# Kernel tuning notes

Measured on AMD Instinct MI355X. Metric: run time of the kernel, lower is better.

## Reference

```python
import jax, jax.numpy as jnp
import numpy as np
from math import comb

B = 1024                 # num_batch
NUM, NVAR, NUM_OBS = 100, 11, 10
T_FIN = 15.0
K_P = 20.0; K_D = 2.0 * np.sqrt(20.0); K_P_V = 20.0
A_OBS, B_OBS = 8.0, 4.2
RHO_V, RHO_PROJ, RHO_LANE, RHO_OBS, RHO_OFFSET, RHO_INEQ = 1.0, 1.0, 100.0, 100.0, 1.0, 100.0
V_MIN, V_MAX, A_MAX = 0.1, 30.0, 8.0
MAXITER = 20
LATENT, HID, INP_DIM, TRAJ_DIM = 2, 1024, 55, 200


def _bernstein():
    # degree-10 Bernstein polynomial basis on [0, T_FIN], sampled at NUM points
    n = NVAR - 1
    s = np.linspace(0.0, 1.0, NUM)
    bm = lambda m: np.stack([comb(m, k) * s**k * (1.0 - s)**(m - k) for k in range(m + 1)], 1)
    P, B9, B8 = bm(n), bm(n - 1), bm(n - 2)
    Z = np.zeros(NUM)
    Pdot = np.stack([(n / T_FIN) * ((B9[:, k - 1] if k >= 1 else Z) - (B9[:, k] if k <= n - 1 else Z)) for k in range(n + 1)], 1)
    Pddot = np.stack([(n * (n - 1) / T_FIN**2) * ((B8[:, k - 2] if k >= 2 else Z) - 2.0 * (B8[:, k - 1] if 1 <= k <= n - 1 else Z) + (B8[:, k] if k <= n - 2 else Z)) for k in range(n + 1)], 1)
    return tuple(jnp.asarray(a, jnp.float32) for a in (P, Pdot, Pddot))


def _forward(inp, initial_state_ego, traj_gt, y_ub, y_lb, eps,
             enc_w1, enc_b1, enc_w2, enc_b2, enc_wmu, enc_bmu, enc_wlv, enc_blv,
             dec_w1, dec_b1, dec_w2, dec_b2, dec_w3, dec_b3,
             P, Pdot, Pddot, inp_mean, inp_std):
    Bn = inp.shape[0]
    tot_time = jnp.linspace(0.0, T_FIN, NUM)

    # ---- cVAE encode / reparameterize / decode ----
    inp_n = (inp - inp_mean) / inp_std
    h = jax.nn.relu(jnp.concatenate([inp_n, traj_gt], 1) @ enc_w1 + enc_b1)
    h = jax.nn.relu(h @ enc_w2 + enc_b2)
    mu = h @ enc_wmu + enc_bmu
    logvar = h @ enc_wlv + enc_blv
    z = mu + jnp.exp(0.5 * logvar) * eps
    h = jax.nn.relu(jnp.concatenate([z, inp_n], 1) @ dec_w1 + dec_b1)
    h = jax.nn.relu(h @ dec_w2 + dec_b2)
    nn_out = h @ dec_w3 + dec_b3          # (B, 8): 4 v_des + 4 y_des setpoints

    # ---- constant constraint matrices ----
    A_eq_x = jnp.stack([P[0], Pdot[0], Pddot[0]])                 # (3, 11)
    A_eq_y = jnp.stack([P[0], Pdot[0], Pddot[0], Pdot[-1]])       # (4, 11)
    A_pd = Pddot - K_P * P - K_D * Pdot
    A_vd = Pddot - K_P_V * Pdot
    cost_smooth = Pddot.T @ Pddot
    I = jnp.eye(NVAR, dtype=P.dtype)

    def kkt_inv(cost, A_eq):
        m = A_eq.shape[0]
        M = jnp.block([[cost, A_eq.T], [A_eq, jnp.zeros((m, m), cost.dtype)]])
        return jnp.linalg.inv(M)

    # ---- boundary conditions ----
    zb = jnp.zeros((Bn,), inp.dtype)
    b_eq_x = jnp.stack([zb, initial_state_ego[:, 2], zb], 1)
    b_eq_y = jnp.stack([zb, initial_state_ego[:, 3], zb, zb], 1)

    # ---- QP layer 1 (behavioral layer) ----
    # sum_i A_vd_i^T A_vd_i over the 4 row-partitions == A_vd^T A_vd
    cost1_x = cost_smooth + RHO_V * (A_vd.T @ A_vd)
    cost1_y = cost_smooth + RHO_OFFSET * (A_pd.T @ A_pd)
    inv1_x = kkt_inv(cost1_x, A_eq_x)
    inv1_y = kkt_inv(cost1_y, A_eq_y)
    v_des = jnp.repeat(nn_out[:, 0:4], NUM // 4, axis=1)   # (B, 100) piecewise setpoints
    y_des = jnp.repeat(nn_out[:, 4:8], NUM // 4, axis=1)
    lincost_x1 = -RHO_V * ((-K_P_V * v_des) @ A_vd)
    lincost_y1 = -RHO_OFFSET * ((-K_P * y_des) @ A_pd)
    c_x_bar = (jnp.concatenate([-lincost_x1, b_eq_x], 1) @ inv1_x.T)[:, :NVAR]
    c_y_bar = (jnp.concatenate([-lincost_y1, b_eq_y], 1) @ inv1_y.T)[:, :NVAR]

    # ---- obstacle constant-velocity rollouts (obstacle-major, matches tile(P)) ----
    x_obs, y_obs = inp[:, 5::5], inp[:, 6::5]
    vx_obs, vy_obs = inp[:, 7::5], inp[:, 8::5]
    x_obs_traj = (x_obs[:, :, None] + vx_obs[:, :, None] * tot_time).reshape(Bn, NUM_OBS * NUM)
    y_obs_traj = (y_obs[:, :, None] + vy_obs[:, :, None] * tot_time).reshape(Bn, NUM_OBS * NUM)

    # ---- QP layer 2 (iterative ADMM-style projection) ----
    A_obs_m = jnp.tile(P, (NUM_OBS, 1))          # (1000, 11)
    A_lane = jnp.vstack([P, -P])                 # (200, 11)
    A_vel, A_acc = Pdot, Pddot
    cost2_x = RHO_PROJ * I + RHO_OBS * (A_obs_m.T @ A_obs_m) + RHO_INEQ * (A_acc.T @ A_acc) + RHO_INEQ * (A_vel.T @ A_vel)
    cost2_y = cost2_x + RHO_LANE * (A_lane.T @ A_lane)
    inv2_x = kkt_inv(cost2_x, A_eq_x)
    inv2_y = kkt_inv(cost2_y, A_eq_y)
    ones_num = jnp.ones((1, NUM), inp.dtype)
    b_lane = jnp.concatenate([y_ub[:, None] * ones_num, -y_lb[:, None] * ones_num], 1)  # (B, 200)

    def step(carry, _):
        primal, lx, ly = carry
        cx, cy = primal[:, :NVAR], primal[:, NVAR:]
        x, xdot, xddot = cx @ P.T, cx @ Pdot.T, cx @ Pddot.T
        y, ydot, yddot = cy @ P.T, cy @ Pdot.T, cy @ Pddot.T
        # obstacle polar decomposition
        wc = jnp.tile(x, (1, NUM_OBS)) - x_obs_traj
        ws = jnp.tile(y, (1, NUM_OBS)) - y_obs_traj
        a_o = jnp.arctan2(A_OBS * ws, B_OBS * wc)
        ca, sa = jnp.cos(a_o), jnp.sin(a_o)
        c1 = RHO_OBS * (A_OBS**2 * ca**2 + B_OBS**2 * sa**2)
        c2 = RHO_OBS * (A_OBS * wc * ca + B_OBS * ws * sa)
        d_o = jnp.maximum(1.0, c2 / c1)
        # velocity / acceleration polar decomposition with box clipping
        a_v = jnp.arctan2(ydot, xdot)
        cv, sv = jnp.cos(a_v), jnp.sin(a_v)
        d_v = jnp.clip(xdot * cv + ydot * sv, V_MIN, V_MAX)
        a_a = jnp.arctan2(yddot, xddot)
        caa, saa = jnp.cos(a_a), jnp.sin(a_a)
        d_a = jnp.clip(xddot * caa + yddot * saa, 0.0, A_MAX)
        # lane slack
        lane_proj = cy @ A_lane.T
        s_lane = jnp.maximum(0.0, b_lane - lane_proj)
        res_lane = lane_proj - b_lane + s_lane
        # residuals -> dual updates
        rxo = wc - A_OBS * d_o * ca
        ryo = ws - B_OBS * d_o * sa
        rvx, rvy = xdot - d_v * cv, ydot - d_v * sv
        rax, ray = xddot - d_a * caa, yddot - d_a * saa
        lx = lx - RHO_OBS * (rxo @ A_obs_m) - RHO_INEQ * (rax @ A_acc) - RHO_INEQ * (rvx @ A_vel)
        ly = ly - RHO_OBS * (ryo @ A_obs_m) - RHO_INEQ * (ray @ A_acc) - RHO_INEQ * (rvy @ A_vel) - RHO_LANE * (res_lane @ A_lane)
        # linear cost + batched KKT solve via precomputed inverse
        b_ox = x_obs_traj + A_OBS * d_o * ca
        b_oy = y_obs_traj + B_OBS * d_o * sa
        lin_x = -lx - RHO_PROJ * c_x_bar - RHO_OBS * (b_ox @ A_obs_m) - RHO_INEQ * ((d_a * caa) @ A_acc) - RHO_INEQ * ((d_v * cv) @ A_vel)
        lin_y = -ly - RHO_PROJ * c_y_bar - RHO_OBS * (b_oy @ A_obs_m) - RHO_INEQ * ((d_a * saa) @ A_acc) - RHO_INEQ * ((d_v * sv) @ A_vel) - RHO_LANE * ((b_lane - s_lane) @ A_lane)
        sx = (jnp.concatenate([-lin_x, b_eq_x], 1) @ inv2_x.T)[:, :NVAR]
        sy = (jnp.concatenate([-lin_y, b_eq_y], 1) @ inv2_y.T)[:, :NVAR]
        return (jnp.concatenate([sx, sy], 1), lx, ly), None

    primal0 = jnp.concatenate([c_x_bar, c_y_bar], 1)
    lam0 = jnp.zeros((Bn, NVAR), inp.dtype)
    (primal, _, _), _ = jax.lax.scan(step, (primal0, lam0, lam0), None, length=MAXITER)
    return primal  # (B, 2*NVAR) projected trajectory coefficients


def setup_inputs() -> dict:
    key = jax.random.key(0)
    ks = jax.random.split(key, 16)
    P, Pdot, Pddot = _bernstein()
    n = lambda k, sh, sc=1.0: sc * jax.random.normal(k, sh, jnp.float32)
    return {
        "inp": n(ks[0], (B, INP_DIM), 5.0),
        "initial_state_ego": jnp.concatenate([jnp.zeros((B, 2), jnp.float32), 10.0 + n(ks[1], (B, 2))], 1),
        "traj_gt": n(ks[2], (B, TRAJ_DIM)),
        "y_ub": jnp.full((B,), 3.5, jnp.float32),
        "y_lb": jnp.full((B,), -3.5, jnp.float32),
        "eps": n(ks[3], (B, LATENT)),
        "enc_w1": n(ks[4], (INP_DIM + TRAJ_DIM, HID), 0.05), "enc_b1": jnp.zeros((HID,), jnp.float32),
        "enc_w2": n(ks[5], (HID, HID), 0.03), "enc_b2": jnp.zeros((HID,), jnp.float32),
        "enc_wmu": n(ks[6], (HID, LATENT), 0.03), "enc_bmu": jnp.zeros((LATENT,), jnp.float32),
        "enc_wlv": n(ks[7], (HID, LATENT), 0.03), "enc_blv": jnp.zeros((LATENT,), jnp.float32),
        "dec_w1": n(ks[8], (LATENT + INP_DIM, HID), 0.05), "dec_b1": jnp.zeros((HID,), jnp.float32),
        "dec_w2": n(ks[9], (HID, HID), 0.03), "dec_b2": jnp.zeros((HID,), jnp.float32),
        "dec_w3": n(ks[10], (HID, 8), 0.03), "dec_b3": jnp.zeros((8,), jnp.float32),
        "P": P, "Pdot": Pdot, "Pddot": Pddot,
        "inp_mean": jnp.zeros((INP_DIM,), jnp.float32),
        "inp_std": jnp.ones((INP_DIM,), jnp.float32),
    }


def reference(inp, initial_state_ego, traj_gt, y_ub, y_lb, eps,
              enc_w1, enc_b1, enc_w2, enc_b2, enc_wmu, enc_bmu, enc_wlv, enc_blv,
              dec_w1, dec_b1, dec_w2, dec_b2, dec_w3, dec_b3,
              P, Pdot, Pddot, inp_mean, inp_std):
    return _forward(inp, initial_state_ego, traj_gt, y_ub, y_lb, eps,
                    enc_w1, enc_b1, enc_w2, enc_b2, enc_wmu, enc_bmu, enc_wlv, enc_blv,
                    dec_w1, dec_b1, dec_w2, dec_b2, dec_w3, dec_b3,
                    P, Pdot, Pddot, inp_mean, inp_std)
```

## Files before the change

### kernel.cpp

```cpp
#include <hip/hip_runtime.h>
#include <hip/hip_bf16.h>
#include <math.h>

#define BATCH   1024
#define NUMPT   100
#define NVAR    11
#define NOBS    10
#define HID     1024
#define INPD    55
#define TRAJD   200

#define T_FIN_C   15.0f
#define K_P_C     20.0f
#define K_D_C     8.944271909999159f
#define K_P_V_C   20.0f
#define A_OBS_C   8.0f
#define B_OBS_C   4.2f
#define AB_C      33.6f
#define ABSQ_C    1128.96f
#define RHO_V_C      1.0f
#define RHO_PROJ_C   1.0f
#define RHO_LANE_C   100.0f
#define RHO_OBS_C    100.0f
#define RHO_OFFSET_C 1.0f
#define RHO_INEQ_C   100.0f
#define V_MIN_C   0.1f
#define V_MAX_C   30.0f
#define A_MAX_C   8.0f
#define MAXIT     20

#define WS_INV1X  0
#define WS_INV1Y  256
#define WS_INV2X  512
#define WS_INV2Y  768
#define WS_SVD    1024
#define WS_SPD    1088
#define WS_QX     1152
#define WS_QY     1280
#define WS_R2X    1408
#define WS_R2Y    1536
#define WS_BIG    2048

typedef __bf16 bf16x8 __attribute__((ext_vector_type(8)));
typedef float  f32x4  __attribute__((ext_vector_type(4)));

__global__ __launch_bounds__(256) void setup_kernel(
    const float* __restrict__ Pg, const float* __restrict__ Pdg,
    const float* __restrict__ Pddg, float* __restrict__ ws,
    const float* __restrict__ inp, const float* __restrict__ traj,
    const float* __restrict__ mean, const float* __restrict__ stdv,
    __bf16* __restrict__ enc_in, __bf16* __restrict__ dec_in,
    const float* __restrict__ w1, const float* __restrict__ w2,
    const float* __restrict__ w3, const float* __restrict__ w4,
    __bf16* __restrict__ o1, __bf16* __restrict__ o2,
    __bf16* __restrict__ o3, __bf16* __restrict__ o4)
{
    __shared__ float sP[NUMPT*NVAR], sPd[NUMPT*NVAR], sPdd[NUMPT*NVAR];
    __shared__ float aug[15][31];
    __shared__ float fcol[15];
    __shared__ float sQ[121];
    __shared__ float sn[INPD];
    __shared__ float tile[64][65];
    __shared__ float s_pivinv;
    __shared__ int   s_pidx;
    const int tid = threadIdx.x, bid = blockIdx.x;

    if (bid >= 1028) {
        const int tb = bid - 1028;
        int wsel, kt, nt;
        if (tb < 64)       { wsel = 0; kt = tb >> 4;        nt = tb & 15; }
        else if (tb < 320) { wsel = 1; kt = (tb-64) >> 4;   nt = (tb-64) & 15; }
        else if (tb < 352) { wsel = 2; kt = (tb-320) >> 4;  nt = (tb-320) & 15; }
        else               { wsel = 3; kt = (tb-352) >> 4;  nt = (tb-352) & 15; }
        const float* W = (wsel==0) ? w1 : (wsel==1) ? w2 : (wsel==2) ? w3 : w4;
        __bf16* O      = (wsel==0) ? o1 : (wsel==1) ? o2 : (wsel==2) ? o3 : o4;
        const int K  = (wsel==0) ? 255 : (wsel==2) ? 57 : 1024;
        const int Kp = (wsel==0) ? 256 : (wsel==2) ? 128 : 1024;
        if (kt*64 >= Kp) return;
        const int k0 = kt*64, n0 = nt*64;
        const int rr = tid >> 6, c = tid & 63;
        #pragma unroll 4
        for (int it = 0; it < 16; ++it) {
            const int r = it*4 + rr;
            tile[r][c] = (k0 + r < K) ? W[(size_t)(k0 + r)*HID + n0 + c] : 0.0f;
        }
        __syncthreads();
        #pragma unroll 4
        for (int it = 0; it < 16; ++it) {
            const int r = it*4 + rr;
            O[(size_t)(n0 + r)*Kp + k0 + c] = (__bf16)tile[c][r];
        }
        return;
    }

    if (bid >= 4) {
        const int b = bid - 4;
        if (tid < INPD) {
            const float v = (inp[b*INPD + tid] - mean[tid]) / stdv[tid];
            sn[tid] = v;
            enc_in[b*256 + tid] = (__bf16)v;
        } else if (tid < 255) {
            enc_in[b*256 + tid] = (__bf16)traj[b*TRAJD + (tid - INPD)];
        } else {
            enc_in[b*256 + 255] = (__bf16)0.0f;
        }
        __syncthreads();
        if (tid >= 2 && tid < 128)
            dec_in[b*128 + tid] = (__bf16)((tid < 57) ? sn[tid - 2] : 0.0f);
        return;
    }

    for (int i = tid; i < NUMPT*NVAR; i += 256) {
        sP[i] = Pg[i]; sPd[i] = Pdg[i]; sPdd[i] = Pddg[i];
    }
    for (int i = tid; i < 15*31; i += 256) (&aug[0][0])[i] = 0.0f;
    __syncthreads();

    const int N = (bid == 0 || bid == 2) ? 14 : 15;

    if (tid < 121) {
        const int i = tid / 11, j = tid % 11;
        float s = 0.0f;
        if (bid == 0) {
            for (int t = 0; t < NUMPT; ++t) {
                float pdd_i = sPdd[t*NVAR+i], pdd_j = sPdd[t*NVAR+j];
                float av_i = pdd_i - K_P_V_C * sPd[t*NVAR+i];
                float av_j = pdd_j - K_P_V_C * sPd[t*NVAR+j];
                s += pdd_i*pdd_j + RHO_V_C * av_i*av_j;
            }
        } else if (bid == 1) {
            for (int t = 0; t < NUMPT; ++t) {
                float pdd_i = sPdd[t*NVAR+i], pdd_j = sPdd[t*NVAR+j];
                float ap_i = pdd_i - K_P_C*sP[t*NVAR+i] - K_D_C*sPd[t*NVAR+i];
                float ap_j = pdd_j - K_P_C*sP[t*NVAR+j] - K_D_C*sPd[t*NVAR+j];
                s += pdd_i*pdd_j + RHO_OFFSET_C * ap_i*ap_j;
            }
        } else {
            float obs_w = RHO_OBS_C * (float)NOBS;
            if (bid == 3) obs_w += RHO_LANE_C * 2.0f;
            for (int t = 0; t < NUMPT; ++t) {
                float p_i = sP[t*NVAR+i],   p_j = sP[t*NVAR+j];
                float pd_i = sPd[t*NVAR+i], pd_j = sPd[t*NVAR+j];
                float pdd_i = sPdd[t*NVAR+i], pdd_j = sPdd[t*NVAR+j];
                s += obs_w*p_i*p_j + RHO_INEQ_C*(pdd_i*pdd_j + pd_i*pd_j);
            }
            if (i == j) s += RHO_PROJ_C;
        }
        aug[i][j] = s;
    }
    if (tid < 11) {
        const int i = tid;
        float a0 = sP[i], a1 = sPd[i], a2 = sPdd[i];
        aug[i][11] = a0; aug[11][i] = a0;
        aug[i][12] = a1; aug[12][i] = a1;
        aug[i][13] = a2; aug[13][i] = a2;
        if (N == 15) { float a3 = sPd[99*NVAR + i]; aug[i][14] = a3; aug[14][i] = a3; }
    }
    if (tid < N) aug[tid][N + tid] = 1.0f;

    if (bid == 0 && tid < 44) {
        const int c = tid / 11, k = tid % 11;
        float sv = 0.0f, sp = 0.0f;
        for (int t = 25*c; t < 25*c + 25; ++t) {
            float p = sP[t*NVAR+k], pd = sPd[t*NVAR+k], pdd = sPdd[t*NVAR+k];
            sv += pdd - K_P_V_C * pd;
            sp += pdd - K_P_C * p - K_D_C * pd;
        }
        ws[WS_SVD + tid] = sv;
        ws[WS_SPD + tid] = sp;
    }
    __syncthreads();

    if ((bid == 2 || bid == 3) && tid < 121) {
        float v = aug[tid/11][tid%11];
        if (tid/11 == tid%11) v -= RHO_PROJ_C;
        sQ[tid] = v;
        ws[(bid == 2 ? WS_QX : WS_QY) + tid] = v;
    }

    for (int k = 0; k < N; ++k) {
        if (tid == 0) {
            int p = k; float best = fabsf(aug[k][k]);
            for (int i = k+1; i < N; ++i) {
                float v = fabsf(aug[i][k]);
                if (v > best) { best = v; p = i; }
            }
            s_pidx = p;
        }
        __syncthreads();
        const int p = s_pidx;
        if (p != k && tid < 2*N) {
            float tmp = aug[k][tid]; aug[k][tid] = aug[p][tid]; aug[p][tid] = tmp;
        }
        __syncthreads();
        if (tid == 0) s_pivinv = 1.0f / aug[k][k];
        __syncthreads();
        if (tid < 2*N) aug[k][tid] *= s_pivinv;
        __syncthreads();
        if (tid < N) fcol[tid] = (tid == k) ? 0.0f : aug[tid][k];
        __syncthreads();
        for (int idx = tid; idx < N*2*N; idx += 256) {
            const int i = idx / (2*N), j = idx % (2*N);
            if (i != k) aug[i][j] = fmaf(-fcol[i], aug[k][j], aug[i][j]);
        }
        __syncthreads();
    }

    float* dst = ws + (bid == 0 ? WS_INV1X : bid == 1 ? WS_INV1Y
                      : bid == 2 ? WS_INV2X : WS_INV2Y);
    for (int idx = tid; idx < N*N; idx += 256)
        dst[idx] = aug[idx / N][N + idx % N];
    __syncthreads();

    if ((bid == 2 || bid == 3) && tid < 121) {
        const int k = tid / 11, j = tid % 11;
        float a = 0.0f;
        #pragma unroll
        for (int m = 0; m < 11; ++m) a = fmaf(aug[k][N + m], sQ[m*11 + j], a);
        ws[(bid == 2 ? WS_R2X : WS_R2Y) + tid] = a;
    }
}

#define GEMM_CORE(A_, Wt_, Kp_, ...)                                          \
    __shared__ __bf16 As[32][136];                                            \
    __shared__ __bf16 Bs[64][136];                                            \
    const int tid = threadIdx.x;                                              \
    const int lane = tid & 63, wv = tid >> 6;                                 \
    const int wm = (wv >> 1) * 16, wn = (wv & 1) * 32;                        \
    const int ln = lane & 15, q = lane >> 4;                                  \
    const int row0 = blockIdx.y * 32, col0 = blockIdx.x * 64;                 \
    const int r16 = tid >> 4, ch = (tid & 15) * 8;                            \
    f32x4 acc0 = (f32x4){0,0,0,0}, acc1 = (f32x4){0,0,0,0};                   \
    for (int k0 = 0; k0 < (Kp_); k0 += 128) {                                 \
        bf16x8 va = *(const bf16x8*)&(A_)[(size_t)(row0 + r16)*(Kp_) + k0 + ch]; \
        bf16x8 vb = *(const bf16x8*)&(A_)[(size_t)(row0 + r16 + 16)*(Kp_) + k0 + ch]; \
        __VA_ARGS__                                                           \
        *(bf16x8*)&As[r16][ch] = va;                                          \
        *(bf16x8*)&As[r16 + 16][ch] = vb;                                     \
        _Pragma("unroll")                                                     \
        for (int p = 0; p < 4; ++p)                                           \
            *(bf16x8*)&Bs[r16 + 16*p][ch] =                                   \
                *(const bf16x8*)&(Wt_)[(size_t)(col0 + r16 + 16*p)*(Kp_) + k0 + ch]; \
        __syncthreads();                                                      \
        _Pragma("unroll")                                                     \
        for (int kc = 0; kc < 4; ++kc) {                                      \
            const bf16x8 a  = *(const bf16x8*)&As[wm + ln][kc*32 + q*8];      \
            const bf16x8 b0 = *(const bf16x8*)&Bs[wn + ln][kc*32 + q*8];      \
            const bf16x8 b1 = *(const bf16x8*)&Bs[wn + 16 + ln][kc*32 + q*8]; \
            acc0 = __builtin_amdgcn_mfma_f32_16x16x32_bf16(a, b0, acc0, 0, 0, 0); \
            acc1 = __builtin_amdgcn_mfma_f32_16x16x32_bf16(a, b1, acc1, 0, 0, 0); \
        }                                                                     \
        __syncthreads();                                                      \
    }

#define GEMM_WRITE_RELU(C_)                                                   \
    _Pragma("unroll")                                                         \
    for (int ni = 0; ni < 2; ++ni) {                                          \
        const int col = col0 + wn + ni*16 + ln;                               \
        const float bv = bias[col];                                           \
        const f32x4 av = ni ? acc1 : acc0;                                    \
        _Pragma("unroll")                                                     \
        for (int r = 0; r < 4; ++r) {                                         \
            const int row = row0 + wm + q*4 + r;                              \
            (C_)[(size_t)row * HID + col] = (__bf16)fmaxf(av[r] + bv, 0.0f);  \
        }                                                                     \
    }

__global__ __launch_bounds__(256) void gemm_relu(
    const __bf16* __restrict__ A, const __bf16* __restrict__ Wt,
    const float* __restrict__ bias, __bf16* __restrict__ C, int Kp)
{
    GEMM_CORE(A, Wt, Kp)
    GEMM_WRITE_RELU(C)
}

__global__ __launch_bounds__(256) void gemm_mulv(
    const __bf16* __restrict__ A, const __bf16* __restrict__ Wt,
    const float* __restrict__ bias,
    const float* __restrict__ wmu, const float* __restrict__ wlv,
    float* __restrict__ pmulv, int Kp)
{
    GEMM_CORE(A, Wt, Kp)
    const int c0 = col0 + wn + ln;
    const int c1 = c0 + 16;
    const float b0v = bias[c0], b1v = bias[c1];
    const float wm00 = wmu[c0*2+0], wm01 = wmu[c0*2+1];
    const float wm10 = wmu[c1*2+0], wm11 = wmu[c1*2+1];
    const float wl00 = wlv[c0*2+0], wl01 = wlv[c0*2+1];
    const float wl10 = wlv[c1*2+0], wl11 = wlv[c1*2+1];
    float pr[4][4];
    #pragma unroll
    for (int r = 0; r < 4; ++r) {
        const float h0 = fmaxf(acc0[r] + b0v, 0.0f);
        const float h1 = fmaxf(acc1[r] + b1v, 0.0f);
        pr[r][0] = fmaf(h0, wm00, h1*wm10);
        pr[r][1] = fmaf(h0, wm01, h1*wm11);
        pr[r][2] = fmaf(h0, wl00, h1*wl10);
        pr[r][3] = fmaf(h0, wl01, h1*wl11);
    }
    #pragma unroll
    for (int m = 1; m <= 8; m <<= 1)
        #pragma unroll
        for (int r = 0; r < 4; ++r)
            #pragma unroll
            for (int j = 0; j < 4; ++j)
                pr[r][j] += __shfl_xor(pr[r][j], m);
    if (ln == 0) {
        const int part = blockIdx.x*2 + (wv & 1);
        #pragma unroll
        for (int r = 0; r < 4; ++r) {
            const int row = row0 + wm + q*4 + r;
            *(float4*)&pmulv[(size_t)row*128 + part*4] =
                make_float4(pr[r][0], pr[r][1], pr[r][2], pr[r][3]);
        }
    }
}

__global__ __launch_bounds__(256) void gemm_zfix(
    const __bf16* __restrict__ A, const __bf16* __restrict__ Wt,
    const float* __restrict__ bias, __bf16* __restrict__ C, int Kp,
    const float* __restrict__ pmulv, const float* __restrict__ bmu,
    const float* __restrict__ blv, const float* __restrict__ eps)
{
    GEMM_CORE(A, Wt, Kp,
        if (ch == 0 && k0 == 0) {
            const int ra = row0 + r16;
            const int rb = ra + 16;
            float4 sa = make_float4(0.0f, 0.0f, 0.0f, 0.0f);
            float4 sb = make_float4(0.0f, 0.0f, 0.0f, 0.0f);
            for (int p = 0; p < 32; ++p) {
                const float4 qa = *(const float4*)&pmulv[(size_t)ra*128 + p*4];
                const float4 qb = *(const float4*)&pmulv[(size_t)rb*128 + p*4];
                sa.x += qa.x; sa.y += qa.y; sa.z += qa.z; sa.w += qa.w;
                sb.x += qb.x; sb.y += qb.y; sb.z += qb.z; sb.w += qb.w;
            }
            va[0] = (__bf16)fmaf(expf(0.5f*(sa.z + blv[0])), eps[ra*2+0], sa.x + bmu[0]);
            va[1] = (__bf16)fmaf(expf(0.5f*(sa.w + blv[1])), eps[ra*2+1], sa.y + bmu[1]);
            vb[0] = (__bf16)fmaf(expf(0.5f*(sb.z + blv[0])), eps[rb*2+0], sb.x + bmu[0]);
            vb[1] = (__bf16)fmaf(expf(0.5f*(sb.w + blv[1])), eps[rb*2+1], sb.y + bmu[1]);
        }
    )
    GEMM_WRITE_RELU(C)
}

__global__ __launch_bounds__(256) void gemm_out8(
    const __bf16* __restrict__ A, const __bf16* __restrict__ Wt,
    const float* __restrict__ bias, const float* __restrict__ w3,
    float* __restrict__ pnn, int Kp)
{
    GEMM_CORE(A, Wt, Kp)
    const int c0 = col0 + wn + ln;
    const int c1 = c0 + 16;
    const float b0v = bias[c0], b1v = bias[c1];
    float pr[4][8];
    #pragma unroll
    for (int r = 0; r < 4; ++r) {
        const float h0 = fmaxf(acc0[r] + b0v, 0.0f);
        const float h1 = fmaxf(acc1[r] + b1v, 0.0f);
        #pragma unroll
        for (int j = 0; j < 8; ++j)
            pr[r][j] = fmaf(h0, w3[c0*8 + j], h1*w3[c1*8 + j]);
    }
    #pragma unroll
    for (int m = 1; m <= 8; m <<= 1)
        #pragma unroll
        for (int r = 0; r < 4; ++r)
            #pragma unroll
            for (int j = 0; j < 8; ++j)
                pr[r][j] += __shfl_xor(pr[r][j], m);
    if (ln == 0) {
        const int part = blockIdx.x*2 + (wv & 1);
        #pragma unroll
        for (int r = 0; r < 4; ++r) {
            const int row = row0 + wm + q*4 + r;
            *(float4*)&pnn[(size_t)row*256 + part*8] =
                make_float4(pr[r][0], pr[r][1], pr[r][2], pr[r][3]);
            *(float4*)&pnn[(size_t)row*256 + part*8 + 4] =
                make_float4(pr[r][4], pr[r][5], pr[r][6], pr[r][7]);
        }
    }
}

#define DOT11(bb, a0, a1, a2) \
    fmaf(bb[0],a0.x, fmaf(bb[1],a0.y, fmaf(bb[2],a0.z, fmaf(bb[3],a0.w, \
    fmaf(bb[4],a1.x, fmaf(bb[5],a1.y, fmaf(bb[6],a1.z, fmaf(bb[7],a1.w, \
    fmaf(bb[8],a2.x, fmaf(bb[9],a2.y, bb[10]*a2.z))))))))))

__global__ __launch_bounds__(256) void solver_kernel(
    const float* __restrict__ pnn, const float* __restrict__ b3,
    const float* __restrict__ inp,
    const float* __restrict__ ise, const float* __restrict__ yub_p,
    const float* __restrict__ ylb_p,
    const float* __restrict__ Pg, const float* __restrict__ Pdg,
    const float* __restrict__ Pddg,
    const float* __restrict__ ws, float* __restrict__ out)
{
    __shared__ __align__(16) float sBcol[3][11][108];
    __shared__ float s_i2x[196], s_i2y[225], sR2x[121], sR2y[121];
    __shared__ __align__(16) float rows[7][104];
    __shared__ float dval[2][80];
    __shared__ __align__(16) float cxs[12], cys[12];
    __shared__ float wlin[24];
    __shared__ float obsS[4][10];
    __shared__ float nnS[8];

    const int tid = threadIdx.x;
    const int e = blockIdx.x;

    for (int i = tid; i < 3*11*108; i += 256) {
        const int mat = i / 1188, rem = i - mat*1188;
        const int k = rem / 108, t = rem - k*108;
        const float* G = (mat == 0) ? Pg : (mat == 1 ? Pdg : Pddg);
        sBcol[mat][k][t] = (t < NUMPT) ? G[t*NVAR + k] : 0.0f;
    }
    for (int i = tid; i < 196; i += 256) s_i2x[i] = ws[WS_INV2X + i];
    for (int i = tid; i < 225; i += 256) s_i2y[i] = ws[WS_INV2Y + i];
    for (int i = tid; i < 121; i += 256) { sR2x[i] = ws[WS_R2X + i]; sR2y[i] = ws[WS_R2Y + i]; }
    if (tid >= 200 && tid < 240) {
        const int i = tid - 200;
        obsS[i/10][i%10] = inp[e*INPD + 5 + (i/10) + 5*(i%10)];
    }
    if (tid >= 240 && tid < 248) {
        const int j = tid - 240;
        float s = b3[j];
        for (int p = 0; p < 32; ++p) s += pnn[(size_t)e*256 + p*8 + j];
        nnS[j] = s;
    }
    if (tid >= 64 && tid < 92) {
        const int i = tid - 64;
        rows[i >> 2][100 + (i & 3)] = 0.0f;
    }
    if (tid == 92) cxs[11] = 0.0f;
    if (tid == 93) cys[11] = 0.0f;

    const bool isA = (tid < 200);
    const int tA = tid >> 1, hA = tid & 1;
    const bool isB = (tid < 154);
    const int hB = (tid >= 77) ? 1 : 0;
    const int dB = tid - 77*hB;
    const int rB = dB / 11, kB = dB - 11*rB;
    const int mB = (rB==1||rB==4) ? 2 : ((rB==2||rB==5) ? 1 : 0);
    const float* colp = &sBcol[mB][kB][hB*52];
    const float* rowp = &rows[rB][hB*52];

    float bP[NVAR], bQ[NVAR];
    if (isA) {
        const float* Qsrc = hA ? Pddg : Pdg;
        #pragma unroll
        for (int k = 0; k < NVAR; ++k) {
            bP[k] = Pg[tA*NVAR+k];
            bQ[k] = Qsrc[tA*NVAR+k];
        }
    }

    const float vx0 = ise[e*4 + 2], vy0 = ise[e*4 + 3];
    const float yub = yub_p[e], ylb = ylb_p[e];
    __syncthreads();

    const float DT = T_FIN_C / 99.0f;
    float xo[5], yo[5];
    if (isA) {
        const int ob0 = 5*hA;
        #pragma unroll
        for (int o = 0; o < 5; ++o) {
            xo[o] = fmaf(obsS[2][ob0+o], tA*DT, obsS[0][ob0+o]);
            yo[o] = fmaf(obsS[3][ob0+o], tA*DT, obsS[1][ob0+o]);
        }
    }

    if (tid < 11) {
        float s = 0;
        #pragma unroll
        for (int c = 0; c < 4; ++c)
            s = fmaf(nnS[c], ws[WS_SVD + c*11 + tid], s);
        wlin[tid] = RHO_V_C * K_P_V_C * s;
    } else if (tid < 22) {
        const int k = tid - 11;
        float s = 0;
        #pragma unroll
        for (int c = 0; c < 4; ++c)
            s = fmaf(nnS[4 + c], ws[WS_SPD + c*11 + k], s);
        wlin[tid] = RHO_OFFSET_C * K_P_C * s;
    }
    __syncthreads();

    float lam = 0.0f, cb = 0.0f;
    if (tid < 11) {
        const int k = tid;
        float a = vx0 * ws[WS_INV1X + k*14 + 12];
        #pragma unroll
        for (int j = 0; j < NVAR; ++j)
            a = fmaf(-wlin[j], ws[WS_INV1X + k*14 + j], a);
        cb = a; cxs[k] = a;
    } else if (tid < 22) {
        const int k = tid - 11;
        float a = vy0 * ws[WS_INV1Y + k*15 + 12];
        #pragma unroll
        for (int j = 0; j < NVAR; ++j)
            a = fmaf(-wlin[11 + j], ws[WS_INV1Y + k*15 + j], a);
        cb = a; cys[k] = a;
    }
    __syncthreads();

    for (int it = 0; it < MAXIT; ++it) {
        if (isA) {
            const float4 x0 = *(const float4*)&cxs[0];
            const float4 x1 = *(const float4*)&cxs[4];
            const float4 x2 = *(const float4*)&cxs[8];
            const float4 y0 = *(const float4*)&cys[0];
            const float4 y1 = *(const float4*)&cys[4];
            const float4 y2 = *(const float4*)&cys[8];
            const float px = DOT11(bP, x0, x1, x2);
            const float py = DOT11(bP, y0, y1, y2);
            const float qx = DOT11(bQ, x0, x1, x2);
            const float qy = DOT11(bQ, y0, y1, y2);

            float srx = 0.0f, sry = 0.0f;
            #pragma unroll
            for (int o = 0; o < 5; ++o) {
                const float wc = px - xo[o], wsv = py - yo[o];
                const float aw = A_OBS_C * wsv, bw = B_OBS_C * wc;
                const float r2 = aw*aw + bw*bw;
                if (r2 > 0.0f) {
                    const float f = (r2 < ABSQ_C) ? (1.0f - AB_C * rsqrtf(r2)) : 0.0f;
                    srx = fmaf(wc, f, srx);
                    sry = fmaf(wsv, f, sry);
                } else {
                    srx -= A_OBS_C;
                }
            }
            const float mrx = srx + __shfl_xor(srx, 1);
            const float mry = sry + __shfl_xor(sry, 1);

            if (hA == 0) {
                rows[0][tA] = mrx;
                rows[3][tA] = mry;
                const float rv2 = qx*qx + qy*qy;
                float vxr, vyr;
                if (rv2 > 0.0f) {
                    const float ri = rsqrtf(rv2);
                    const float dv = fminf(fmaxf(rv2*ri, V_MIN_C), V_MAX_C);
                    const float f = 1.0f - dv*ri;
                    vxr = qx*f; vyr = qy*f;
                } else { vxr = -V_MIN_C; vyr = 0.0f; }
                rows[2][tA] = vxr;  rows[5][tA] = vyr;
                rows[6][tA] = fmaxf(0.0f, py - yub) - fmaxf(0.0f, ylb - py);
            } else {
                const float ra2 = qx*qx + qy*qy;
                float axr = 0.0f, ayr = 0.0f;
                if (ra2 > A_MAX_C*A_MAX_C) {
                    const float ri = rsqrtf(ra2);
                    const float f = 1.0f - A_MAX_C*ri;
                    axr = qx*f; ayr = qy*f;
                }
                rows[1][tA] = axr;  rows[4][tA] = ayr;
            }
        }
        __syncthreads();

        if (isB) {
            float s0 = 0.0f, s1 = 0.0f;
            #pragma unroll
            for (int i = 0; i < 13; ++i) {
                const float4 rr = *(const float4*)&rowp[i*4];
                const float4 cc = *(const float4*)&colp[i*4];
                s0 = fmaf(rr.x, cc.x, s0); s1 = fmaf(rr.y, cc.y, s1);
                s0 = fmaf(rr.z, cc.z, s0); s1 = fmaf(rr.w, cc.w, s1);
            }
            dval[hB][dB] = s0 + s1;
        }
        __syncthreads();

        if (tid < 22) {
            const int k = (tid < 11) ? tid : tid - 11;
            float u;
            if (tid < 11)
                u = RHO_OBS_C * ((dval[0][k]      + dval[1][k])
                               + (dval[0][11 + k] + dval[1][11 + k])
                               + (dval[0][22 + k] + dval[1][22 + k]));
            else
                u = RHO_OBS_C * ((dval[0][33 + k] + dval[1][33 + k])
                               + (dval[0][44 + k] + dval[1][44 + k])
                               + (dval[0][55 + k] + dval[1][55 + k])
                               + (dval[0][66 + k] + dval[1][66 + k]));
            wlin[tid] = 2.0f*u - lam - cb;
            lam -= u;
        }
        __builtin_amdgcn_wave_barrier();
        if (tid < 22) {
            const int k = (tid < 11) ? tid : tid - 11;
            if (tid < 11) {
                float a = vx0 * s_i2x[k*14 + 12];
                #pragma unroll
                for (int j = 0; j < NVAR; ++j) {
                    a = fmaf(-wlin[j], s_i2x[k*14 + j], a);
                    a = fmaf(sR2x[k*11 + j], cxs[j], a);
                }
                cxs[k] = a;
            } else {
                float a = vy0 * s_i2y[k*15 + 12];
                #pragma unroll
                for (int j = 0; j < NVAR; ++j) {
                    a = fmaf(-wlin[11 + j], s_i2y[k*15 + j], a);
                    a = fmaf(sR2y[k*11 + j], cys[j], a);
                }
                cys[k] = a;
            }
        }
        __syncthreads();
    }

    if (tid < NVAR) {
        out[e*22 + tid]      = cxs[tid];
        out[e*22 + 11 + tid] = cys[tid];
    }
}

extern "C" void kernel_launch(void* const* d_in, const int* in_sizes, int n_in,
                              void* d_out, int out_size, void* d_ws, size_t ws_size,
                              hipStream_t stream)
{
    (void)in_sizes; (void)n_in; (void)out_size; (void)ws_size;
    const float* inp    = (const float*)d_in[0];
    const float* ise    = (const float*)d_in[1];
    const float* traj   = (const float*)d_in[2];
    const float* yub    = (const float*)d_in[3];
    const float* ylb    = (const float*)d_in[4];
    const float* eps    = (const float*)d_in[5];
    const float* enc_w1 = (const float*)d_in[6];
    const float* enc_b1 = (const float*)d_in[7];
    const float* enc_w2 = (const float*)d_in[8];
    const float* enc_b2 = (const float*)d_in[9];
    const float* wmu    = (const float*)d_in[10];
    const float* bmu    = (const float*)d_in[11];
    const float* wlv    = (const float*)d_in[12];
    const float* blv    = (const float*)d_in[13];
    const float* dec_w1 = (const float*)d_in[14];
    const float* dec_b1 = (const float*)d_in[15];
    const float* dec_w2 = (const float*)d_in[16];
    const float* dec_b2 = (const float*)d_in[17];
    const float* dec_w3 = (const float*)d_in[18];
    const float* dec_b3 = (const float*)d_in[19];
    const float* P      = (const float*)d_in[20];
    const float* Pd     = (const float*)d_in[21];
    const float* Pdd    = (const float*)d_in[22];
    const float* mean   = (const float*)d_in[23];
    const float* stdv   = (const float*)d_in[24];

    float* ws    = (float*)d_ws;
    float* pmulv = ws + WS_BIG;
    float* pnn   = pmulv + (size_t)BATCH*128;
    __bf16* bfb  = (__bf16*)(pnn + (size_t)BATCH*256);
    __bf16* enc_in = bfb;
    __bf16* dec_in = enc_in + (size_t)BATCH*256;
    __bf16* hA     = dec_in + (size_t)BATCH*128;
    __bf16* wt1    = hA + (size_t)BATCH*HID;
    __bf16* wt2    = wt1 + (size_t)HID*256;
    __bf16* wt3    = wt2 + (size_t)HID*HID;
    __bf16* wt4    = wt3 + (size_t)HID*128;
    float* outf = (float*)d_out;

    setup_kernel<<<4 + 1024 + 608, 256, 0, stream>>>(
        P, Pd, Pdd, ws, inp, traj, mean, stdv, enc_in, dec_in,
        enc_w1, enc_w2, dec_w1, dec_w2, wt1, wt2, wt3, wt4);

    dim3 g(16, 32);
    gemm_relu<<<g, 256, 0, stream>>>(enc_in, wt1, enc_b1, hA, 256);
    gemm_mulv<<<g, 256, 0, stream>>>(hA, wt2, enc_b2, wmu, wlv, pmulv, 1024);
    gemm_zfix<<<g, 256, 0, stream>>>(dec_in, wt3, dec_b1, hA, 128,
                                     pmulv, bmu, blv, eps);
    gemm_out8<<<g, 256, 0, stream>>>(hA, wt4, dec_b2, dec_w3, pnn, 1024);
    solver_kernel<<<BATCH, 256, 0, stream>>>(pnn, dec_b3, inp, ise, yub, ylb,
                                             P, Pd, Pdd, ws, outf);
}
```

Measured before the change: 218.2 us.

## Fuse setup and four GEMM kernels into one persistent kernel with grid barriers

Merges the setup kernel (constant KKT inverses, input normalization, weight transposes) and the four MLP GEMM launches into a single 512-block persistent kernel. Stages are separated by atomic-counter grid barriers, and the counters are reset by a memset before launch. This removes kernel launch gaps and tail effects between the small stages. In exchange it relies on all 512 blocks being co-resident to avoid deadlock, and adds spin-wait barrier overhead.

```diff
diff --git a/kernel.cpp b/kernel.cpp
--- a/kernel.cpp
+++ b/kernel.cpp
@@ -39,197 +39,27 @@
 #define WS_QY     1280
 #define WS_R2X    1408
 #define WS_R2Y    1536
+#define WS_CTR    1700
 #define WS_BIG    2048
 
 typedef __bf16 bf16x8 __attribute__((ext_vector_type(8)));
 typedef float  f32x4  __attribute__((ext_vector_type(4)));
 
-__global__ __launch_bounds__(256) void setup_kernel(
-    const float* __restrict__ Pg, const float* __restrict__ Pdg,
-    const float* __restrict__ Pddg, float* __restrict__ ws,
-    const float* __restrict__ inp, const float* __restrict__ traj,
-    const float* __restrict__ mean, const float* __restrict__ stdv,
-    __bf16* __restrict__ enc_in, __bf16* __restrict__ dec_in,
-    const float* __restrict__ w1, const float* __restrict__ w2,
-    const float* __restrict__ w3, const float* __restrict__ w4,
-    __bf16* __restrict__ o1, __bf16* __restrict__ o2,
-    __bf16* __restrict__ o3, __bf16* __restrict__ o4)
-{
-    __shared__ float sP[NUMPT*NVAR], sPd[NUMPT*NVAR], sPdd[NUMPT*NVAR];
-    __shared__ float aug[15][31];
-    __shared__ float fcol[15];
-    __shared__ float sQ[121];
-    __shared__ float sn[INPD];
-    __shared__ float tile[64][65];
-    __shared__ float s_pivinv;
-    __shared__ int   s_pidx;
-    const int tid = threadIdx.x, bid = blockIdx.x;
-
-    if (bid >= 1028) {
-        const int tb = bid - 1028;
-        int wsel, kt, nt;
-        if (tb < 64)       { wsel = 0; kt = tb >> 4;        nt = tb & 15; }
-        else if (tb < 320) { wsel = 1; kt = (tb-64) >> 4;   nt = (tb-64) & 15; }
-        else if (tb < 352) { wsel = 2; kt = (tb-320) >> 4;  nt = (tb-320) & 15; }
-        else               { wsel = 3; kt = (tb-352) >> 4;  nt = (tb-352) & 15; }
-        const float* W = (wsel==0) ? w1 : (wsel==1) ? w2 : (wsel==2) ? w3 : w4;
-        __bf16* O      = (wsel==0) ? o1 : (wsel==1) ? o2 : (wsel==2) ? o3 : o4;
-        const int K  = (wsel==0) ? 255 : (wsel==2) ? 57 : 1024;
-        const int Kp = (wsel==0) ? 256 : (wsel==2) ? 128 : 1024;
-        if (kt*64 >= Kp) return;
-        const int k0 = kt*64, n0 = nt*64;
-        const int rr = tid >> 6, c = tid & 63;
-        #pragma unroll 4
-        for (int it = 0; it < 16; ++it) {
-            const int r = it*4 + rr;
-            tile[r][c] = (k0 + r < K) ? W[(size_t)(k0 + r)*HID + n0 + c] : 0.0f;
-        }
-        __syncthreads();
-        #pragma unroll 4
-        for (int it = 0; it < 16; ++it) {
-            const int r = it*4 + rr;
-            O[(size_t)(n0 + r)*Kp + k0 + c] = (__bf16)tile[c][r];
-        }
-        return;
-    }
-
-    if (bid >= 4) {
-        const int b = bid - 4;
-        if (tid < INPD) {
-            const float v = (inp[b*INPD + tid] - mean[tid]) / stdv[tid];
-            sn[tid] = v;
-            enc_in[b*256 + tid] = (__bf16)v;
-        } else if (tid < 255) {
-            enc_in[b*256 + tid] = (__bf16)traj[b*TRAJD + (tid - INPD)];
-        } else {
-            enc_in[b*256 + 255] = (__bf16)0.0f;
-        }
-        __syncthreads();
-        if (tid >= 2 && tid < 128)
-            dec_in[b*128 + tid] = (__bf16)((tid < 57) ? sn[tid - 2] : 0.0f);
-        return;
-    }
-
-    for (int i = tid; i < NUMPT*NVAR; i += 256) {
-        sP[i] = Pg[i]; sPd[i] = Pdg[i]; sPdd[i] = Pddg[i];
-    }
-    for (int i = tid; i < 15*31; i += 256) (&aug[0][0])[i] = 0.0f;
+#define NBLK 512
+
+__device__ __forceinline__ void gbar(int* ctr, int s) {
     __syncthreads();
-
-    const int N = (bid == 0 || bid == 2) ? 14 : 15;
-
-    if (tid < 121) {
-        const int i = tid / 11, j = tid % 11;
-        float s = 0.0f;
-        if (bid == 0) {
-            for (int t = 0; t < NUMPT; ++t) {
-                float pdd_i = sPdd[t*NVAR+i], pdd_j = sPdd[t*NVAR+j];
-                float av_i = pdd_i - K_P_V_C * sPd[t*NVAR+i];
-                float av_j = pdd_j - K_P_V_C * sPd[t*NVAR+j];
-                s += pdd_i*pdd_j + RHO_V_C * av_i*av_j;
-            }
-        } else if (bid == 1) {
-            for (int t = 0; t < NUMPT; ++t) {
-                float pdd_i = sPdd[t*NVAR+i], pdd_j = sPdd[t*NVAR+j];
-                float ap_i = pdd_i - K_P_C*sP[t*NVAR+i] - K_D_C*sPd[t*NVAR+i];
-                float ap_j = pdd_j - K_P_C*sP[t*NVAR+j] - K_D_C*sPd[t*NVAR+j];
-                s += pdd_i*pdd_j + RHO_OFFSET_C * ap_i*ap_j;
-            }
-        } else {
-            float obs_w = RHO_OBS_C * (float)NOBS;
-            if (bid == 3) obs_w += RHO_LANE_C * 2.0f;
-            for (int t = 0; t < NUMPT; ++t) {
-                float p_i = sP[t*NVAR+i],   p_j = sP[t*NVAR+j];
-                float pd_i = sPd[t*NVAR+i], pd_j = sPd[t*NVAR+j];
-                float pdd_i = sPdd[t*NVAR+i], pdd_j = sPdd[t*NVAR+j];
-                s += obs_w*p_i*p_j + RHO_INEQ_C*(pdd_i*pdd_j + pd_i*pd_j);
-            }
-            if (i == j) s += RHO_PROJ_C;
-        }
-        aug[i][j] = s;
-    }
-    if (tid < 11) {
-        const int i = tid;
-        float a0 = sP[i], a1 = sPd[i], a2 = sPdd[i];
-        aug[i][11] = a0; aug[11][i] = a0;
-        aug[i][12] = a1; aug[12][i] = a1;
-        aug[i][13] = a2; aug[13][i] = a2;
-        if (N == 15) { float a3 = sPd[99*NVAR + i]; aug[i][14] = a3; aug[14][i] = a3; }
-    }
-    if (tid < N) aug[tid][N + tid] = 1.0f;
-
-    if (bid == 0 && tid < 44) {
-        const int c = tid / 11, k = tid % 11;
-        float sv = 0.0f, sp = 0.0f;
-        for (int t = 25*c; t < 25*c + 25; ++t) {
-            float p = sP[t*NVAR+k], pd = sPd[t*NVAR+k], pdd = sPdd[t*NVAR+k];
-            sv += pdd - K_P_V_C * pd;
-            sp += pdd - K_P_C * p - K_D_C * pd;
-        }
-        ws[WS_SVD + tid] = sv;
-        ws[WS_SPD + tid] = sp;
+    if (threadIdx.x == 0) {
+        __hip_atomic_fetch_add(&ctr[s], 1, __ATOMIC_ACQ_REL,
+                               __HIP_MEMORY_SCOPE_AGENT);
+        while (__hip_atomic_load(&ctr[s], __ATOMIC_ACQUIRE,
+                                 __HIP_MEMORY_SCOPE_AGENT) < NBLK)
+            __builtin_amdgcn_s_sleep(1);
     }
     __syncthreads();
-
-    if ((bid == 2 || bid == 3) && tid < 121) {
-        float v = aug[tid/11][tid%11];
-        if (tid/11 == tid%11) v -= RHO_PROJ_C;
-        sQ[tid] = v;
-        ws[(bid == 2 ? WS_QX : WS_QY) + tid] = v;
-    }
-
-    for (int k = 0; k < N; ++k) {
-        if (tid == 0) {
-            int p = k; float best = fabsf(aug[k][k]);
-            for (int i = k+1; i < N; ++i) {
-                float v = fabsf(aug[i][k]);
-                if (v > best) { best = v; p = i; }
-            }
-            s_pidx = p;
-        }
-        __syncthreads();
-        const int p = s_pidx;
-        if (p != k && tid < 2*N) {
-            float tmp = aug[k][tid]; aug[k][tid] = aug[p][tid]; aug[p][tid] = tmp;
-        }
-        __syncthreads();
-        if (tid == 0) s_pivinv = 1.0f / aug[k][k];
-        __syncthreads();
-        if (tid < 2*N) aug[k][tid] *= s_pivinv;
-        __syncthreads();
-        if (tid < N) fcol[tid] = (tid == k) ? 0.0f : aug[tid][k];
-        __syncthreads();
-        for (int idx = tid; idx < N*2*N; idx += 256) {
-            const int i = idx / (2*N), j = idx % (2*N);
-            if (i != k) aug[i][j] = fmaf(-fcol[i], aug[k][j], aug[i][j]);
-        }
-        __syncthreads();
-    }
-
-    float* dst = ws + (bid == 0 ? WS_INV1X : bid == 1 ? WS_INV1Y
-                      : bid == 2 ? WS_INV2X : WS_INV2Y);
-    for (int idx = tid; idx < N*N; idx += 256)
-        dst[idx] = aug[idx / N][N + idx % N];
-    __syncthreads();
-
-    if ((bid == 2 || bid == 3) && tid < 121) {
-        const int k = tid / 11, j = tid % 11;
-        float a = 0.0f;
-        #pragma unroll
-        for (int m = 0; m < 11; ++m) a = fmaf(aug[k][N + m], sQ[m*11 + j], a);
-        ws[(bid == 2 ? WS_R2X : WS_R2Y) + tid] = a;
-    }
 }
 
-#define GEMM_CORE(A_, Wt_, Kp_, ...)                                          \
-    __shared__ __bf16 As[32][136];                                            \
-    __shared__ __bf16 Bs[64][136];                                            \
-    const int tid = threadIdx.x;                                              \
-    const int lane = tid & 63, wv = tid >> 6;                                 \
-    const int wm = (wv >> 1) * 16, wn = (wv & 1) * 32;                        \
-    const int ln = lane & 15, q = lane >> 4;                                  \
-    const int row0 = blockIdx.y * 32, col0 = blockIdx.x * 64;                 \
-    const int r16 = tid >> 4, ch = (tid & 15) * 8;                            \
+#define MEGA_GEMM(A_, Wt_, Kp_, ...)                                          \
     f32x4 acc0 = (f32x4){0,0,0,0}, acc1 = (f32x4){0,0,0,0};                   \
     for (int k0 = 0; k0 < (Kp_); k0 += 128) {                                 \
         bf16x8 va = *(const bf16x8*)&(A_)[(size_t)(row0 + r16)*(Kp_) + k0 + ch]; \
@@ -253,130 +83,323 @@
         __syncthreads();                                                      \
     }
 
-#define GEMM_WRITE_RELU(C_)                                                   \
-    _Pragma("unroll")                                                         \
-    for (int ni = 0; ni < 2; ++ni) {                                          \
-        const int col = col0 + wn + ni*16 + ln;                               \
-        const float bv = bias[col];                                           \
-        const f32x4 av = ni ? acc1 : acc0;                                    \
-        _Pragma("unroll")                                                     \
-        for (int r = 0; r < 4; ++r) {                                         \
-            const int row = row0 + wm + q*4 + r;                              \
-            (C_)[(size_t)row * HID + col] = (__bf16)fmaxf(av[r] + bv, 0.0f);  \
-        }                                                                     \
-    }
-
-__global__ __launch_bounds__(256) void gemm_relu(
-    const __bf16* __restrict__ A, const __bf16* __restrict__ Wt,
-    const float* __restrict__ bias, __bf16* __restrict__ C, int Kp)
+__global__ __launch_bounds__(256) void mega_kernel(
+    const float* __restrict__ Pg, const float* __restrict__ Pdg,
+    const float* __restrict__ Pddg, float* __restrict__ ws,
+    const float* __restrict__ inp, const float* __restrict__ traj,
+    const float* __restrict__ mean, const float* __restrict__ stdv,
+    __bf16* __restrict__ enc_in, __bf16* __restrict__ dec_in,
+    const float* __restrict__ w1, const float* __restrict__ w2,
+    const float* __restrict__ w3, const float* __restrict__ w4,
+    __bf16* __restrict__ o1, __bf16* __restrict__ o2,
+    __bf16* __restrict__ o3, __bf16* __restrict__ o4,
+    const float* __restrict__ b1, const float* __restrict__ b2,
+    const float* __restrict__ bd1, const float* __restrict__ bd2,
+    const float* __restrict__ wmu, const float* __restrict__ wlv,
+    const float* __restrict__ bmu, const float* __restrict__ blv,
+    const float* __restrict__ eps, const float* __restrict__ w3o,
+    __bf16* __restrict__ hA, float* __restrict__ pmulv,
+    float* __restrict__ pnn, int* __restrict__ ctr)
 {
-    GEMM_CORE(A, Wt, Kp)
-    GEMM_WRITE_RELU(C)
-}
-
-__global__ __launch_bounds__(256) void gemm_mulv(
-    const __bf16* __restrict__ A, const __bf16* __restrict__ Wt,
-    const float* __restrict__ bias,
-    const float* __restrict__ wmu, const float* __restrict__ wlv,
-    float* __restrict__ pmulv, int Kp)
-{
-    GEMM_CORE(A, Wt, Kp)
-    const int c0 = col0 + wn + ln;
-    const int c1 = c0 + 16;
-    const float b0v = bias[c0], b1v = bias[c1];
-    const float wm00 = wmu[c0*2+0], wm01 = wmu[c0*2+1];
-    const float wm10 = wmu[c1*2+0], wm11 = wmu[c1*2+1];
-    const float wl00 = wlv[c0*2+0], wl01 = wlv[c0*2+1];
-    const float wl10 = wlv[c1*2+0], wl11 = wlv[c1*2+1];
-    float pr[4][4];
-    #pragma unroll
-    for (int r = 0; r < 4; ++r) {
-        const float h0 = fmaxf(acc0[r] + b0v, 0.0f);
-        const float h1 = fmaxf(acc1[r] + b1v, 0.0f);
-        pr[r][0] = fmaf(h0, wm00, h1*wm10);
-        pr[r][1] = fmaf(h0, wm01, h1*wm11);
-        pr[r][2] = fmaf(h0, wl00, h1*wl10);
-        pr[r][3] = fmaf(h0, wl01, h1*wl11);
-    }
-    #pragma unroll
-    for (int m = 1; m <= 8; m <<= 1)
-        #pragma unroll
-        for (int r = 0; r < 4; ++r)
-            #pragma unroll
-            for (int j = 0; j < 4; ++j)
-                pr[r][j] += __shfl_xor(pr[r][j], m);
-    if (ln == 0) {
-        const int part = blockIdx.x*2 + (wv & 1);
+    __shared__ __align__(16) char smem[26112];
+    __bf16 (*As)[136] = (__bf16(*)[136])smem;
+    __bf16 (*Bs)[136] = (__bf16(*)[136])(smem + 8704);
+
+    const int tid = threadIdx.x, bid = blockIdx.x;
+    const int lane = tid & 63, wv = tid >> 6;
+    const int wm = (wv >> 1) * 16, wn = (wv & 1) * 32;
+    const int ln = lane & 15, q = lane >> 4;
+    const int row0 = (bid >> 4) * 32, col0 = (bid & 15) * 64;
+    const int r16 = tid >> 4, ch = (tid & 15) * 8;
+
+    if (bid < 4) {
+        float* sP   = (float*)smem;
+        float* sPd  = sP + 1100;
+        float* sPdd = sPd + 1100;
+        float (*aug)[31] = (float(*)[31])(sPdd + 1100);
+        float* fcol = (float*)aug + 465;
+        float* sQv  = fcol + 16;
+        float* s_piv = sQv + 124;
+        int*   s_pid = (int*)(s_piv + 1);
+
+        for (int i = tid; i < NUMPT*NVAR; i += 256) {
+            sP[i] = Pg[i]; sPd[i] = Pdg[i]; sPdd[i] = Pddg[i];
+        }
+        for (int i = tid; i < 15*31; i += 256) ((float*)aug)[i] = 0.0f;
+        __syncthreads();
+
+        const int N = (bid == 0 || bid == 2) ? 14 : 15;
+
+        if (tid < 121) {
+            const int i = tid / 11, j = tid % 11;
+            float s = 0.0f;
+            if (bid == 0) {
+                for (int t = 0; t < NUMPT; ++t) {
+                    float pdd_i = sPdd[t*NVAR+i], pdd_j = sPdd[t*NVAR+j];
+                    float av_i = pdd_i - K_P_V_C * sPd[t*NVAR+i];
+                    float av_j = pdd_j - K_P_V_C * sPd[t*NVAR+j];
+                    s += pdd_i*pdd_j + RHO_V_C * av_i*av_j;
+                }
+            } else if (bid == 1) {
+                for (int t = 0; t < NUMPT; ++t) {
+                    float pdd_i = sPdd[t*NVAR+i], pdd_j = sPdd[t*NVAR+j];
+                    float ap_i = pdd_i - K_P_C*sP[t*NVAR+i] - K_D_C*sPd[t*NVAR+i];
+                    float ap_j = pdd_j - K_P_C*sP[t*NVAR+j] - K_D_C*sPd[t*NVAR+j];
+                    s += pdd_i*pdd_j + RHO_OFFSET_C * ap_i*ap_j;
+                }
+            } else {
+                float obs_w = RHO_OBS_C * (float)NOBS;
+                if (bid == 3) obs_w += RHO_LANE_C * 2.0f;
+                for (int t = 0; t < NUMPT; ++t) {
+                    float p_i = sP[t*NVAR+i],   p_j = sP[t*NVAR+j];
+                    float pd_i = sPd[t*NVAR+i], pd_j = sPd[t*NVAR+j];
+                    float pdd_i = sPdd[t*NVAR+i], pdd_j = sPdd[t*NVAR+j];
+                    s += obs_w*p_i*p_j + RHO_INEQ_C*(pdd_i*pdd_j + pd_i*pd_j);
+                }
+                if (i == j) s += RHO_PROJ_C;
+            }
+            aug[i][j] = s;
+        }
+        if (tid < 11) {
+            const int i = tid;
+            float a0 = sP[i], a1 = sPd[i], a2 = sPdd[i];
+            aug[i][11] = a0; aug[11][i] = a0;
+            aug[i][12] = a1; aug[12][i] = a1;
+            aug[i][13] = a2; aug[13][i] = a2;
+            if (N == 15) { float a3 = sPd[99*NVAR + i]; aug[i][14] = a3; aug[14][i] = a3; }
+        }
+        if (tid < N) aug[tid][N + tid] = 1.0f;
+
+        if (bid == 0 && tid < 44) {
+            const int c = tid / 11, k = tid % 11;
+            float sv = 0.0f, sp = 0.0f;
+            for (int t = 25*c; t < 25*c + 25; ++t) {
+                float p = sP[t*NVAR+k], pd = sPd[t*NVAR+k], pdd = sPdd[t*NVAR+k];
+                sv += pdd - K_P_V_C * pd;
+                sp += pdd - K_P_C * p - K_D_C * pd;
+            }
+            ws[WS_SVD + tid] = sv;
+            ws[WS_SPD + tid] = sp;
+        }
+        __syncthreads();
+
+        if ((bid == 2 || bid == 3) && tid < 121) {
+            float v = aug[tid/11][tid%11];
+            if (tid/11 == tid%11) v -= RHO_PROJ_C;
+            sQv[tid] = v;
+            ws[(bid == 2 ? WS_QX : WS_QY) + tid] = v;
+        }
+        __syncthreads();
+
+        for (int k = 0; k < N; ++k) {
+            if (tid == 0) {
+                int p = k; float best = fabsf(aug[k][k]);
+                for (int i = k+1; i < N; ++i) {
+                    float v = fabsf(aug[i][k]);
+                    if (v > best) { best = v; p = i; }
+                }
+                *s_pid = p;
+            }
+            __syncthreads();
+            const int p = *s_pid;
+            if (p != k && tid < 2*N) {
+                float tmp = aug[k][tid]; aug[k][tid] = aug[p][tid]; aug[p][tid] = tmp;
+            }
+            __syncthreads();
+            if (tid == 0) *s_piv = 1.0f / aug[k][k];
+            __syncthreads();
+            if (tid < 2*N) aug[k][tid] *= *s_piv;
+            __syncthreads();
+            if (tid < N) fcol[tid] = (tid == k) ? 0.0f : aug[tid][k];
+            __syncthreads();
+            for (int idx = tid; idx < N*2*N; idx += 256) {
+                const int i = idx / (2*N), j = idx % (2*N);
+                if (i != k) aug[i][j] = fmaf(-fcol[i], aug[k][j], aug[i][j]);
+            }
+            __syncthreads();
+        }
+
+        float* dst = ws + (bid == 0 ? WS_INV1X : bid == 1 ? WS_INV1Y
+                          : bid == 2 ? WS_INV2X : WS_INV2Y);
+        for (int idx = tid; idx < N*N; idx += 256)
+            dst[idx] = aug[idx / N][N + idx % N];
+        __syncthreads();
+
+        if ((bid == 2 || bid == 3) && tid < 121) {
+            const int k = tid / 11, j = tid % 11;
+            float a = 0.0f;
+            #pragma unroll
+            for (int m = 0; m < 11; ++m) a = fmaf(aug[k][N + m], sQv[m*11 + j], a);
+            ws[(bid == 2 ? WS_R2X : WS_R2Y) + tid] = a;
+        }
+    } else {
+        float (*tile)[65] = (float(*)[65])smem;
+        for (int item = bid - 4; item < 1632; item += NBLK - 4) {
+            if (item < 608) {
+                int wsel, kt, nt;
+                if (item < 64)       { wsel = 0; kt = item >> 4;       nt = item & 15; }
+                else if (item < 320) { wsel = 1; kt = (item-64) >> 4;  nt = (item-64) & 15; }
+                else if (item < 352) { wsel = 2; kt = (item-320) >> 4; nt = (item-320) & 15; }
+                else                 { wsel = 3; kt = (item-352) >> 4; nt = (item-352) & 15; }
+                const float* W = (wsel==0) ? w1 : (wsel==1) ? w2 : (wsel==2) ? w3 : w4;
+                __bf16* O      = (wsel==0) ? o1 : (wsel==1) ? o2 : (wsel==2) ? o3 : o4;
+                const int K  = (wsel==0) ? 255 : (wsel==2) ? 57 : 1024;
+                const int Kp = (wsel==0) ? 256 : (wsel==2) ? 128 : 1024;
+                if (kt*64 < Kp) {
+                    const int k0 = kt*64, n0 = nt*64;
+                    const int rr = tid >> 6, c = tid & 63;
+                    #pragma unroll 4
+                    for (int it = 0; it < 16; ++it) {
+                        const int r = it*4 + rr;
+                        tile[r][c] = (k0 + r < K) ? W[(size_t)(k0 + r)*HID + n0 + c] : 0.0f;
+                    }
+                    __syncthreads();
+                    #pragma unroll 4
+                    for (int it = 0; it < 16; ++it) {
+                        const int r = it*4 + rr;
+                        O[(size_t)(n0 + r)*Kp + k0 + c] = (__bf16)tile[c][r];
+                    }
+                    __syncthreads();
+                }
+            } else {
+                const int b = item - 608;
+                if (tid < INPD) {
+                    const float v = (inp[b*INPD + tid] - mean[tid]) / stdv[tid];
+                    enc_in[b*256 + tid] = (__bf16)v;
+                } else if (tid < 255) {
+                    enc_in[b*256 + tid] = (__bf16)traj[b*TRAJD + (tid - INPD)];
+                } else {
+                    enc_in[b*256 + 255] = (__bf16)0.0f;
+                }
+                if (tid < 128) {
+                    float dv = 0.0f;
+                    if (tid >= 2 && tid < 57)
+                        dv = (inp[b*INPD + tid - 2] - mean[tid - 2]) / stdv[tid - 2];
+                    dec_in[b*128 + tid] = (__bf16)dv;
+                }
+            }
+        }
+    }
+    gbar(ctr, 0);
+
+    {
+        MEGA_GEMM(enc_in, o1, 256)
+        #pragma unroll
+        for (int ni = 0; ni < 2; ++ni) {
+            const int col = col0 + wn + ni*16 + ln;
+            const float bv = b1[col];
+            const f32x4 av = ni ? acc1 : acc0;
+            #pragma unroll
+            for (int r = 0; r < 4; ++r) {
+                const int row = row0 + wm + q*4 + r;
+                hA[(size_t)row * HID + col] = (__bf16)fmaxf(av[r] + bv, 0.0f);
+            }
+        }
+    }
+    gbar(ctr, 1);
+
+    {
+        MEGA_GEMM(hA, o2, 1024)
+        const int c0 = col0 + wn + ln;
+        const int c1 = c0 + 16;
+        const float b0v = b2[c0], b1v = b2[c1];
+        const float wm00 = wmu[c0*2+0], wm01 = wmu[c0*2+1];
+        const float wm10 = wmu[c1*2+0], wm11 = wmu[c1*2+1];
+        const float wl00 = wlv[c0*2+0], wl01 = wlv[c0*2+1];
+        const float wl10 = wlv[c1*2+0], wl11 = wlv[c1*2+1];
+        float pr[4][4];
         #pragma unroll
         for (int r = 0; r < 4; ++r) {
-            const int row = row0 + wm + q*4 + r;
-            *(float4*)&pmulv[(size_t)row*128 + part*4] =
-                make_float4(pr[r][0], pr[r][1], pr[r][2], pr[r][3]);
-        }
-    }
-}
-
-__global__ __launch_bounds__(256) void gemm_zfix(
-    const __bf16* __restrict__ A, const __bf16* __restrict__ Wt,
-    const float* __restrict__ bias, __bf16* __restrict__ C, int Kp,
-    const float* __restrict__ pmulv, const float* __restrict__ bmu,
-    const float* __restrict__ blv, const float* __restrict__ eps)
-{
-    GEMM_CORE(A, Wt, Kp,
-        if (ch == 0 && k0 == 0) {
-            const int ra = row0 + r16;
-            const int rb = ra + 16;
-            float4 sa = make_float4(0.0f, 0.0f, 0.0f, 0.0f);
-            float4 sb = make_float4(0.0f, 0.0f, 0.0f, 0.0f);
-            for (int p = 0; p < 32; ++p) {
-                const float4 qa = *(const float4*)&pmulv[(size_t)ra*128 + p*4];
-                const float4 qb = *(const float4*)&pmulv[(size_t)rb*128 + p*4];
-                sa.x += qa.x; sa.y += qa.y; sa.z += qa.z; sa.w += qa.w;
-                sb.x += qb.x; sb.y += qb.y; sb.z += qb.z; sb.w += qb.w;
-            }
-            va[0] = (__bf16)fmaf(expf(0.5f*(sa.z + blv[0])), eps[ra*2+0], sa.x + bmu[0]);
-            va[1] = (__bf16)fmaf(expf(0.5f*(sa.w + blv[1])), eps[ra*2+1], sa.y + bmu[1]);
-            vb[0] = (__bf16)fmaf(expf(0.5f*(sb.z + blv[0])), eps[rb*2+0], sb.x + bmu[0]);
-            vb[1] = (__bf16)fmaf(expf(0.5f*(sb.w + blv[1])), eps[rb*2+1], sb.y + bmu[1]);
-        }
-    )
-    GEMM_WRITE_RELU(C)
-}
-
-__global__ __launch_bounds__(256) void gemm_out8(
-    const __bf16* __restrict__ A, const __bf16* __restrict__ Wt,
-    const float* __restrict__ bias, const float* __restrict__ w3,
-    float* __restrict__ pnn, int Kp)
-{
-    GEMM_CORE(A, Wt, Kp)
-    const int c0 = col0 + wn + ln;
-    const int c1 = c0 + 16;
-    const float b0v = bias[c0], b1v = bias[c1];
-    float pr[4][8];
-    #pragma unroll
-    for (int r = 0; r < 4; ++r) {
-        const float h0 = fmaxf(acc0[r] + b0v, 0.0f);
-        const float h1 = fmaxf(acc1[r] + b1v, 0.0f);
-        #pragma unroll
-        for (int j = 0; j < 8; ++j)
-            pr[r][j] = fmaf(h0, w3[c0*8 + j], h1*w3[c1*8 + j]);
-    }
-    #pragma unroll
-    for (int m = 1; m <= 8; m <<= 1)
-        #pragma unroll
-        for (int r = 0; r < 4; ++r)
+            const float h0 = fmaxf(acc0[r] + b0v, 0.0f);
+            const float h1 = fmaxf(acc1[r] + b1v, 0.0f);
+            pr[r][0] = fmaf(h0, wm00, h1*wm10);
+            pr[r][1] = fmaf(h0, wm01, h1*wm11);
+            pr[r][2] = fmaf(h0, wl00, h1*wl10);
+            pr[r][3] = fmaf(h0, wl01, h1*wl11);
+        }
+        #pragma unroll
+        for (int m = 1; m <= 8; m <<= 1)
+            #pragma unroll
+            for (int r = 0; r < 4; ++r)
+                #pragma unroll
+                for (int j = 0; j < 4; ++j)
+                    pr[r][j] += __shfl_xor(pr[r][j], m);
+        if (ln == 0) {
+            const int part = (bid & 15)*2 + (wv & 1);
+            #pragma unroll
+            for (int r = 0; r < 4; ++r) {
+                const int row = row0 + wm + q*4 + r;
+                *(float4*)&pmulv[(size_t)row*128 + part*4] =
+                    make_float4(pr[r][0], pr[r][1], pr[r][2], pr[r][3]);
+            }
+        }
+    }
+    gbar(ctr, 2);
+
+    {
+        MEGA_GEMM(dec_in, o3, 128,
+            if (ch == 0 && k0 == 0) {
+                const int ra = row0 + r16;
+                const int rb = ra + 16;
+                float4 sa = make_float4(0.0f, 0.0f, 0.0f, 0.0f);
+                float4 sb = make_float4(0.0f, 0.0f, 0.0f, 0.0f);
+                for (int p = 0; p < 32; ++p) {
+                    const float4 qa = *(const float4*)&pmulv[(size_t)ra*128 + p*4];
+                    const float4 qb = *(const float4*)&pmulv[(size_t)rb*128 + p*4];
+                    sa.x += qa.x; sa.y += qa.y; sa.z += qa.z; sa.w += qa.w;
+                    sb.x += qb.x; sb.y += qb.y; sb.z += qb.z; sb.w += qb.w;
+                }
+                va[0] = (__bf16)fmaf(expf(0.5f*(sa.z + blv[0])), eps[ra*2+0], sa.x + bmu[0]);
+                va[1] = (__bf16)fmaf(expf(0.5f*(sa.w + blv[1])), eps[ra*2+1], sa.y + bmu[1]);
+                vb[0] = (__bf16)fmaf(expf(0.5f*(sb.z + blv[0])), eps[rb*2+0], sb.x + bmu[0]);
+                vb[1] = (__bf16)fmaf(expf(0.5f*(sb.w + blv[1])), eps[rb*2+1], sb.y + bmu[1]);
+            }
+        )
+        #pragma unroll
+        for (int ni = 0; ni < 2; ++ni) {
+            const int col = col0 + wn + ni*16 + ln;
+            const float bv = bd1[col];
+            const f32x4 av = ni ? acc1 : acc0;
+            #pragma unroll
+            for (int r = 0; r < 4; ++r) {
+                const int row = row0 + wm + q*4 + r;
+                hA[(size_t)row * HID + col] = (__bf16)fmaxf(av[r] + bv, 0.0f);
+            }
+        }
+    }
+    gbar(ctr, 3);
+
+    {
+        MEGA_GEMM(hA, o4, 1024)
+        const int c0 = col0 + wn + ln;
+        const int c1 = c0 + 16;
+        const float b0v = bd2[c0], b1v = bd2[c1];
+        float pr[4][8];
+        #pragma unroll
+        for (int r = 0; r < 4; ++r) {
+            const float h0 = fmaxf(acc0[r] + b0v, 0.0f);
+            const float h1 = fmaxf(acc1[r] + b1v, 0.0f);
             #pragma unroll
             for (int j = 0; j < 8; ++j)
-                pr[r][j] += __shfl_xor(pr[r][j], m);
-    if (ln == 0) {
-        const int part = blockIdx.x*2 + (wv & 1);
-        #pragma unroll
-        for (int r = 0; r < 4; ++r) {
-            const int row = row0 + wm + q*4 + r;
-            *(float4*)&pnn[(size_t)row*256 + part*8] =
-                make_float4(pr[r][0], pr[r][1], pr[r][2], pr[r][3]);
-            *(float4*)&pnn[(size_t)row*256 + part*8 + 4] =
-                make_float4(pr[r][4], pr[r][5], pr[r][6], pr[r][7]);
+                pr[r][j] = fmaf(h0, w3o[c0*8 + j], h1*w3o[c1*8 + j]);
+        }
+        #pragma unroll
+        for (int m = 1; m <= 8; m <<= 1)
+            #pragma unroll
+            for (int r = 0; r < 4; ++r)
+                #pragma unroll
+                for (int j = 0; j < 8; ++j)
+                    pr[r][j] += __shfl_xor(pr[r][j], m);
+        if (ln == 0) {
+            const int part = (bid & 15)*2 + (wv & 1);
+            #pragma unroll
+            for (int r = 0; r < 4; ++r) {
+                const int row = row0 + wm + q*4 + r;
+                *(float4*)&pnn[(size_t)row*256 + part*8] =
+                    make_float4(pr[r][0], pr[r][1], pr[r][2], pr[r][3]);
+                *(float4*)&pnn[(size_t)row*256 + part*8 + 4] =
+                    make_float4(pr[r][4], pr[r][5], pr[r][6], pr[r][7]);
+            }
         }
     }
 }
@@ -434,7 +457,7 @@
     if (tid == 93) cys[11] = 0.0f;
 
     const bool isA = (tid < 200);
-    const int tA = tid >> 1, hA = tid & 1;
+    const int tA = tid >> 1, hA2 = tid & 1;
     const bool isB = (tid < 154);
     const int hB = (tid >= 77) ? 1 : 0;
     const int dB = tid - 77*hB;
@@ -445,7 +468,7 @@
 
     float bP[NVAR], bQ[NVAR];
     if (isA) {
-        const float* Qsrc = hA ? Pddg : Pdg;
+        const float* Qsrc = hA2 ? Pddg : Pdg;
         #pragma unroll
         for (int k = 0; k < NVAR; ++k) {
             bP[k] = Pg[tA*NVAR+k];
@@ -460,7 +483,7 @@
     const float DT = T_FIN_C / 99.0f;
     float xo[5], yo[5];
     if (isA) {
-        const int ob0 = 5*hA;
+        const int ob0 = 5*hA2;
         #pragma unroll
         for (int o = 0; o < 5; ++o) {
             xo[o] = fmaf(obsS[2][ob0+o], tA*DT, obsS[0][ob0+o]);
@@ -532,7 +555,7 @@
             const float mrx = srx + __shfl_xor(srx, 1);
             const float mry = sry + __shfl_xor(sry, 1);
 
-            if (hA == 0) {
+            if (hA2 == 0) {
                 rows[0][tA] = mrx;
                 rows[3][tA] = mry;
                 const float rv2 = qx*qx + qy*qy;
@@ -648,6 +671,7 @@
     const float* stdv   = (const float*)d_in[24];
 
     float* ws    = (float*)d_ws;
+    int*   ctr   = (int*)(ws + WS_CTR);
     float* pmulv = ws + WS_BIG;
     float* pnn   = pmulv + (size_t)BATCH*128;
     __bf16* bfb  = (__bf16*)(pnn + (size_t)BATCH*256);
@@ -660,16 +684,14 @@
     __bf16* wt4    = wt3 + (size_t)HID*128;
     float* outf = (float*)d_out;
 
-    setup_kernel<<<4 + 1024 + 608, 256, 0, stream>>>(
+    hipMemsetAsync(ctr, 0, 4*sizeof(int), stream);
+
+    mega_kernel<<<NBLK, 256, 0, stream>>>(
         P, Pd, Pdd, ws, inp, traj, mean, stdv, enc_in, dec_in,
-        enc_w1, enc_w2, dec_w1, dec_w2, wt1, wt2, wt3, wt4);
-
-    dim3 g(16, 32);
-    gemm_relu<<<g, 256, 0, stream>>>(enc_in, wt1, enc_b1, hA, 256);
-    gemm_mulv<<<g, 256, 0, stream>>>(hA, wt2, enc_b2, wmu, wlv, pmulv, 1024);
-    gemm_zfix<<<g, 256, 0, stream>>>(dec_in, wt3, dec_b1, hA, 128,
-                                     pmulv, bmu, blv, eps);
-    gemm_out8<<<g, 256, 0, stream>>>(hA, wt4, dec_b2, dec_w3, pnn, 1024);
+        enc_w1, enc_w2, dec_w1, dec_w2, wt1, wt2, wt3, wt4,
+        enc_b1, enc_b2, dec_b1, dec_b2, wmu, wlv, bmu, blv, eps, dec_w3,
+        hA, pmulv, pnn, ctr);
+
     solver_kernel<<<BATCH, 256, 0, stream>>>(pnn, dec_b3, inp, ise, yub, ylb,
                                              P, Pd, Pdd, ws, outf);
 }
```

After: 392.6 us. 1.8x slower.
